# Performance work log

Measured on AMD Instinct MI355X. Metric: run time of the kernel, lower is better.

## Reference

```python
import jax, jax.numpy as jnp
import numpy as np

N = 25000        # nodes
E = 400000       # edges (before self-loops)
HEADS = 8
GROUPS = 8
F_IN = 256
HID = 64
N_CLASS = 32
N_LAYERS = 3


def grouped_linear(x, w, b):
    # x: [..., Cin], w: [G, Cin//G, Cout//G], b: [Cout]
    G = w.shape[0]
    xs = x.reshape(x.shape[:-1] + (G, -1))
    out = jnp.einsum('...gi,gio->...go', xs, w)
    return out.reshape(x.shape[:-1] + (-1,)) + b


def gcn_norm(edge_index, n):
    # PyG gcn_norm with add_self_loops=True, unit edge weights
    row = jnp.concatenate([edge_index[0], jnp.arange(n)])
    col = jnp.concatenate([edge_index[1], jnp.arange(n)])
    w = jnp.ones(row.shape[0], jnp.float32)
    deg = jax.ops.segment_sum(w, col, num_segments=n)
    dis = jnp.where(deg > 0, jax.lax.rsqrt(deg), 0.0)
    return row, col, dis[row] * w * dis[col]


def dna_conv(x_all, row, col, norm, wq, bq, wk, bk, wv, bv):
    # x_all: [N, L, H]; row/col/norm: [E'] (edges incl. self-loops)
    Ee = row.shape[0]
    L, H = x_all.shape[1], x_all.shape[2]
    dh = H // HEADS
    # query from target's latest state, key/value from full source history
    q = grouped_linear(x_all[col, -1:], wq, bq).reshape(Ee, 1, HEADS, dh).transpose(0, 2, 1, 3)
    k = grouped_linear(x_all[row], wk, bk).reshape(Ee, L, HEADS, dh).transpose(0, 2, 1, 3)
    v = grouped_linear(x_all[row], wv, bv).reshape(Ee, L, HEADS, dh).transpose(0, 2, 1, 3)
    attn = jax.nn.softmax(jnp.einsum('ehqd,ehld->ehql', q, k) / jnp.sqrt(jnp.float32(dh)), axis=-1)
    out = jnp.einsum('ehql,ehld->ehqd', attn, v)           # [E', HEADS, 1, dh]
    out = out.transpose(0, 2, 1, 3).reshape(Ee, H)          # [E', H]
    return jax.ops.segment_sum(norm[:, None] * out, col, num_segments=N)


def setup_inputs() -> dict:
    key = jax.random.key(0)
    ks = jax.random.split(key, 12)
    s = 0.2
    return {
        'x': jax.random.normal(ks[0], (N, F_IN), jnp.float32),
        'edge_index': jax.random.randint(ks[1], (2, E), 0, N),
        'lin1_w': jax.random.normal(ks[2], (F_IN, HID), jnp.float32) * 0.05,
        'lin1_b': jnp.zeros((HID,), jnp.float32),
        'wq': jax.random.normal(ks[3], (N_LAYERS, GROUPS, HID // GROUPS, HID // GROUPS), jnp.float32) * s,
        'bq': jnp.zeros((N_LAYERS, HID), jnp.float32),
        'wk': jax.random.normal(ks[4], (N_LAYERS, GROUPS, HID // GROUPS, HID // GROUPS), jnp.float32) * s,
        'bk': jnp.zeros((N_LAYERS, HID), jnp.float32),
        'wv': jax.random.normal(ks[5], (N_LAYERS, GROUPS, HID // GROUPS, HID // GROUPS), jnp.float32) * s,
        'bv': jnp.zeros((N_LAYERS, HID), jnp.float32),
        'lin2_w': jax.random.normal(ks[6], (HID, N_CLASS), jnp.float32) * 0.1,
        'lin2_b': jnp.zeros((N_CLASS,), jnp.float32),
    }


def reference(x, edge_index, lin1_w, lin1_b, wq, bq, wk, bk, wv, bv, lin2_w, lin2_b):
    row, col, norm = gcn_norm(edge_index, N)
    h = jax.nn.relu(x @ lin1_w + lin1_b)                    # [N, HID]; dropout = identity (eval)
    x_all = h[:, None, :]                                   # [N, 1, HID]
    for l in range(N_LAYERS):
        out = jax.nn.relu(dna_conv(x_all, row, col, norm,
                                   wq[l], bq[l], wk[l], bk[l], wv[l], bv[l]))
        x_all = jnp.concatenate([x_all, out[:, None, :]], axis=1)
    logits = x_all[:, -1] @ lin2_w + lin2_b                 # [N, N_CLASS]
    return jax.nn.log_softmax(logits, axis=1)
```

## Files before the change

kernel.cpp:

```cpp
#include <hip/hip_runtime.h>
#include <hip/hip_fp16.h>
#include <math.h>

#define NN 25000
#define NE 400000
#define HID 64
#define F_IN 256
#define N_CLASS 32
#define MAXL 4
#define KVS 3
#define WPAD 264
#define SCAN_NB 98

typedef _Float16 f16;
typedef _Float16 f16x2 __attribute__((ext_vector_type(2)));
typedef _Float16 f16x8 __attribute__((ext_vector_type(8)));
typedef float f32x4 __attribute__((ext_vector_type(4)));

union F16x8 {
    f16x8 v;
    f16x2 h[4];
    __half2 hh[4];
};

__device__ __forceinline__ float dot2(f16x2 a, f16x2 b, float c) {
#if __has_builtin(__builtin_amdgcn_fdot2)
    return __builtin_amdgcn_fdot2(a, b, c, false);
#else
    return c + (float)a[0] * (float)b[0] + (float)a[1] * (float)b[1];
#endif
}

__global__ void deg_kernel(const int* __restrict__ col, int* __restrict__ deg, int E) {
    int e = blockIdx.x * blockDim.x + threadIdx.x;
    if (e < E) atomicAdd(&deg[col[e]], 1);
}

__global__ void scanA_kernel(const int* __restrict__ deg, int* __restrict__ bsum, int n) {
    int t = threadIdx.x;
    int i = blockIdx.x * 256 + t;
    int v = (i < n) ? deg[i] : 0;
    #pragma unroll
    for (int off = 1; off < 64; off <<= 1) v += __shfl_xor(v, off);
    __shared__ int wsum[4];
    if ((t & 63) == 0) wsum[t >> 6] = v;
    __syncthreads();
    if (t == 0) bsum[blockIdx.x] = wsum[0] + wsum[1] + wsum[2] + wsum[3];
}

__global__ void scanB_kernel(int* __restrict__ bsum, int nb) {
    __shared__ int s[128];
    int t = threadIdx.x;
    int v = (t < nb) ? bsum[t] : 0;
    s[t] = v;
    __syncthreads();
    for (int off = 1; off < 128; off <<= 1) {
        int u = (t >= off) ? s[t - off] : 0;
        __syncthreads();
        s[t] += u;
        __syncthreads();
    }
    if (t < nb) bsum[t] = s[t] - v;
}

__global__ void scanC_kernel(const int* __restrict__ deg, const int* __restrict__ bsum,
                             int* __restrict__ rowptr, int* __restrict__ cursor,
                             float* __restrict__ dis, int n) {
    int t = threadIdx.x;
    int i = blockIdx.x * 256 + t;
    int lane = t & 63, w = t >> 6;
    int v = (i < n) ? deg[i] : 0;
    int x = v;
    #pragma unroll
    for (int off = 1; off < 64; off <<= 1) {
        int u = __shfl_up(x, off);
        if (lane >= off) x += u;
    }
    __shared__ int wsum[4];
    if (lane == 63) wsum[w] = x;
    __syncthreads();
    int base = bsum[blockIdx.x];
    for (int ww = 0; ww < w; ++ww) base += wsum[ww];
    if (i < n) {
        int excl = base + x - v;
        rowptr[i] = excl;
        cursor[i] = excl;
        dis[i] = rsqrtf((float)(v + 1));
    }
}

__global__ void scatter_kernel(const int* __restrict__ row, const int* __restrict__ col,
                               int* __restrict__ cursor, int* __restrict__ csr_src, int E) {
    int e = blockIdx.x * blockDim.x + threadIdx.x;
    if (e >= E) return;
    int c = col[e];
    int p = atomicAdd(&cursor[c], 1);
    csr_src[p] = row[e];
}

__global__ void wprep_kernel(const float* __restrict__ w, f16* __restrict__ wt) {
    int e = blockIdx.x * blockDim.x + threadIdx.x;
    int k = e >> 6, nn = e & 63;
    wt[nn * F_IN + k] = (f16)w[e];
}

__global__ void __launch_bounds__(256) lin1_mfma_kernel(
        const float* __restrict__ x, const f16x8* __restrict__ wt,
        const float* __restrict__ b, float* __restrict__ x_all, int n) {
    __shared__ f16 wlds[64 * WPAD];
    int t = threadIdx.x;
    #pragma unroll
    for (int j = 0; j < 8; ++j) {
        int idx = t + j * 256;
        int e = idx * 8;
        int nr = e >> 8, k0 = e & 255;
        *(f16x8*)&wlds[nr * WPAD + k0] = wt[idx];
    }
    __syncthreads();
    int wave = t >> 6, lane = t & 63;
    int m = lane & 15, quad = lane >> 4;
    int rowA = blockIdx.x * 64 + wave * 16 + m;
    int rA = min(rowA, n - 1);
    const float* xp = x + (size_t)rA * F_IN + quad * 8;
    f32x4 acc[4] = {};
    for (int kk = 0; kk < F_IN; kk += 32) {
        float4 x0 = *(const float4*)(xp + kk);
        float4 x1 = *(const float4*)(xp + kk + 4);
        f16x8 a;
        a[0] = (f16)x0.x; a[1] = (f16)x0.y; a[2] = (f16)x0.z; a[3] = (f16)x0.w;
        a[4] = (f16)x1.x; a[5] = (f16)x1.y; a[6] = (f16)x1.z; a[7] = (f16)x1.w;
        #pragma unroll
        for (int nt = 0; nt < 4; ++nt) {
            f16x8 bf = *(const f16x8*)&wlds[(nt * 16 + m) * WPAD + kk + quad * 8];
            acc[nt] = __builtin_amdgcn_mfma_f32_16x16x32_f16(a, bf, acc[nt], 0, 0, 0);
        }
    }
    int rowC = blockIdx.x * 64 + wave * 16 + quad * 4;
    #pragma unroll
    for (int nt = 0; nt < 4; ++nt) {
        int col = nt * 16 + m;
        float bias = b[col];
        #pragma unroll
        for (int r = 0; r < 4; ++r) {
            int row = rowC + r;
            if (row < n)
                x_all[(size_t)row * (MAXL * HID) + col] = fmaxf(acc[nt][r] + bias, 0.f);
        }
    }
}

__global__ void transform_kernel(const float* __restrict__ x_all,
                                 const float* __restrict__ wq, const float* __restrict__ bq,
                                 const float* __restrict__ wk, const float* __restrict__ bk,
                                 const float* __restrict__ wv, const float* __restrict__ bv,
                                 f16x2* __restrict__ Q2, f16x2* __restrict__ KV,
                                 int n, int L) {
    int t = blockIdx.x * blockDim.x + threadIdx.x;
    int node = t >> 5, u = t & 31;
    if (node >= n) return;
    int g = u >> 2;
    int o0 = (u & 3) * 2;
    const float* xrow = x_all + (size_t)node * (MAXL * HID);

    {
        const float* xg = xrow + (L - 1) * HID + g * 8;
        const float* wg = wq + g * 64;
        float a0 = bq[g * 8 + o0], a1 = bq[g * 8 + o0 + 1];
        #pragma unroll
        for (int i = 0; i < 8; ++i) {
            float xv = xg[i];
            a0 = fmaf(xv, wg[i * 8 + o0], a0);
            a1 = fmaf(xv, wg[i * 8 + o0 + 1], a1);
        }
        f16x2 q; q[0] = (f16)a0; q[1] = (f16)a1;
        Q2[(size_t)node * 32 + u] = q;
    }
    for (int ll = 0; ll < L; ++ll) {
        const float* xg = xrow + ll * HID + g * 8;
        const float* wgk = wk + g * 64;
        const float* wgv = wv + g * 64;
        float k0 = bk[g * 8 + o0], k1 = bk[g * 8 + o0 + 1];
        float v0 = bv[g * 8 + o0], v1 = bv[g * 8 + o0 + 1];
        #pragma unroll
        for (int i = 0; i < 8; ++i) {
            float xv = xg[i];
            k0 = fmaf(xv, wgk[i * 8 + o0], k0);
            k1 = fmaf(xv, wgk[i * 8 + o0 + 1], k1);
            v0 = fmaf(xv, wgv[i * 8 + o0], v0);
            v1 = fmaf(xv, wgv[i * 8 + o0 + 1], v1);
        }
        f16x2 kh; kh[0] = (f16)k0; kh[1] = (f16)k1;
        f16x2 vh; vh[0] = (f16)v0; vh[1] = (f16)v1;
        size_t base = ((size_t)node * KVS + ll) * 2;
        KV[(base + 0) * 32 + u] = kh;
        KV[(base + 1) * 32 + u] = vh;
    }
}

template <int L>
__global__ void gather_kernel(const int* __restrict__ rowptr, const int* __restrict__ deg,
                              const int* __restrict__ csr_src, const float* __restrict__ dis,
                              const f16x8* __restrict__ Q8, const f16x8* __restrict__ KV8,
                              float* __restrict__ x_all, int n) {
    int wave = (int)((blockIdx.x * (size_t)blockDim.x + threadIdx.x) >> 6);
    int lane = threadIdx.x & 63;
    if (wave >= n) return;
    int c = wave;
    int u = lane & 7;
    int slot = lane >> 3;
    F16x8 q; q.v = Q8[(size_t)c * 8 + u];
    float nc = dis[c];
    int beg = rowptr[c];
    int dc = deg[c] + 1;
    float acc[8];
    #pragma unroll
    for (int i = 0; i < 8; ++i) acc[i] = 0.f;

    for (int j = 0; j < dc; j += 8) {
        int jj = j + slot;
        bool valid = jj < dc;
        int r = c;
        if (valid && jj > 0) r = csr_src[beg + jj - 1];
        float nrm = valid ? nc * dis[r] : 0.f;

        F16x8 kk[L], vv[L];
        size_t rb = (size_t)r * (KVS * 2 * 8);
        #pragma unroll
        for (int ll = 0; ll < L; ++ll) {
            kk[ll].v = KV8[rb + ll * 16 + u];
            vv[ll].v = KV8[rb + ll * 16 + 8 + u];
        }
        float s[L];
        #pragma unroll
        for (int ll = 0; ll < L; ++ll) {
            float p = 0.f;
            #pragma unroll
            for (int i2 = 0; i2 < 4; ++i2) p = dot2(q.h[i2], kk[ll].h[i2], p);
            s[ll] = p * 0.35355339059327373f;
        }
        float m = s[0];
        #pragma unroll
        for (int ll = 1; ll < L; ++ll) m = fmaxf(m, s[ll]);
        float sum = 0.f;
        #pragma unroll
        for (int ll = 0; ll < L; ++ll) { s[ll] = __expf(s[ll] - m); sum += s[ll]; }
        float inv = nrm / sum;

        __half2 ha[4];
        #pragma unroll
        for (int i2 = 0; i2 < 4; ++i2) ha[i2] = __float2half2_rn(0.f);
        #pragma unroll
        for (int ll = 0; ll < L; ++ll) {
            __half2 p2 = __float2half2_rn(s[ll] * inv);
            #pragma unroll
            for (int i2 = 0; i2 < 4; ++i2) ha[i2] = __hfma2(p2, vv[ll].hh[i2], ha[i2]);
        }
        #pragma unroll
        for (int i2 = 0; i2 < 4; ++i2) {
            float2 f = __half22float2(ha[i2]);
            acc[i2 * 2]     += f.x;
            acc[i2 * 2 + 1] += f.y;
        }
    }
    #pragma unroll
    for (int off = 8; off < 64; off <<= 1) {
        #pragma unroll
        for (int i = 0; i < 8; ++i) acc[i] += __shfl_xor(acc[i], off);
    }
    if (slot == 0) {
        float4* dst = (float4*)(x_all + ((size_t)c * MAXL + L) * HID + u * 8);
        dst[0] = make_float4(fmaxf(acc[0], 0.f), fmaxf(acc[1], 0.f),
                             fmaxf(acc[2], 0.f), fmaxf(acc[3], 0.f));
        dst[1] = make_float4(fmaxf(acc[4], 0.f), fmaxf(acc[5], 0.f),
                             fmaxf(acc[6], 0.f), fmaxf(acc[7], 0.f));
    }
}

__global__ void final_kernel(const float* __restrict__ x_all, const float* __restrict__ w2,
                             const float* __restrict__ b2, float* __restrict__ out, int n) {
    int t = blockIdx.x * blockDim.x + threadIdx.x;
    int node = t >> 5;
    int o = t & 31;
    if (node >= n) return;
    const float* xr = x_all + (size_t)node * (MAXL * HID) + 3 * HID;
    float logit = b2[o];
    #pragma unroll
    for (int d = 0; d < HID; ++d) logit = fmaf(xr[d], w2[d * N_CLASS + o], logit);
    float m = logit;
    for (int off = 16; off; off >>= 1) m = fmaxf(m, __shfl_xor(m, off, 32));
    float e = expf(logit - m);
    float sum = e;
    for (int off = 16; off; off >>= 1) sum += __shfl_xor(sum, off, 32);
    out[(size_t)node * N_CLASS + o] = (logit - m) - logf(sum);
}

extern "C" void kernel_launch(void* const* d_in, const int* in_sizes, int n_in,
                              void* d_out, int out_size, void* d_ws, size_t ws_size,
                              hipStream_t stream) {
    const float* x      = (const float*)d_in[0];
    const int*   eidx   = (const int*)d_in[1];
    const float* lin1_w = (const float*)d_in[2];
    const float* lin1_b = (const float*)d_in[3];
    const float* wq     = (const float*)d_in[4];
    const float* bq     = (const float*)d_in[5];
    const float* wk     = (const float*)d_in[6];
    const float* bk     = (const float*)d_in[7];
    const float* wv     = (const float*)d_in[8];
    const float* bv     = (const float*)d_in[9];
    const float* lin2_w = (const float*)d_in[10];
    const float* lin2_b = (const float*)d_in[11];
    float* out = (float*)d_out;

    const int n  = NN;
    const int E  = NE;
    const int* row = eidx;
    const int* col = eidx + E;

    char* ws = (char*)d_ws;
    float*  x_all  = (float*)ws;   ws += (size_t)NN * MAXL * HID * 4;
    f16x2*  Q2     = (f16x2*)ws;   ws += (size_t)NN * 32 * 4;
    f16x2*  KV     = (f16x2*)ws;   ws += (size_t)NN * KVS * 2 * 32 * 4;
    float*  dis    = (float*)ws;   ws += (size_t)NN * 4;
    int*    deg    = (int*)ws;     ws += (size_t)NN * 4;
    int*    rowptr = (int*)ws;     ws += (size_t)NN * 4;
    int*    cursor = (int*)ws;     ws += (size_t)NN * 4;
    int*    csr    = (int*)ws;     ws += (size_t)NE * 4;
    f16*    wt16   = (f16*)ws;     ws += (size_t)HID * F_IN * 2;
    int*    bsum   = (int*)ws;     ws += 128 * 4;

    hipMemsetAsync(deg, 0, (size_t)NN * 4, stream);
    deg_kernel<<<(E + 255) / 256, 256, 0, stream>>>(col, deg, E);
    scanA_kernel<<<SCAN_NB, 256, 0, stream>>>(deg, bsum, n);
    scanB_kernel<<<1, 128, 0, stream>>>(bsum, SCAN_NB);
    scanC_kernel<<<SCAN_NB, 256, 0, stream>>>(deg, bsum, rowptr, cursor, dis, n);
    scatter_kernel<<<(E + 255) / 256, 256, 0, stream>>>(row, col, cursor, csr, E);
    wprep_kernel<<<(HID * F_IN + 255) / 256, 256, 0, stream>>>(lin1_w, wt16);

    lin1_mfma_kernel<<<(n + 63) / 64, 256, 0, stream>>>(x, (const f16x8*)wt16, lin1_b, x_all, n);

    for (int l = 0; l < 3; ++l) {
        int L = l + 1;
        transform_kernel<<<(n * 32 + 255) / 256, 256, 0, stream>>>(
            x_all, wq + l * 512, bq + l * 64, wk + l * 512, bk + l * 64,
            wv + l * 512, bv + l * 64, Q2, KV, n, L);
        int blocks = (n + 3) / 4;
        if (L == 1)      gather_kernel<1><<<blocks, 256, 0, stream>>>(rowptr, deg, csr, dis, (const f16x8*)Q2, (const f16x8*)KV, x_all, n);
        else if (L == 2) gather_kernel<2><<<blocks, 256, 0, stream>>>(rowptr, deg, csr, dis, (const f16x8*)Q2, (const f16x8*)KV, x_all, n);
        else             gather_kernel<3><<<blocks, 256, 0, stream>>>(rowptr, deg, csr, dis, (const f16x8*)Q2, (const f16x8*)KV, x_all, n);
    }

    final_kernel<<<(n * N_CLASS + 255) / 256, 256, 0, stream>>>(x_all, lin2_w, lin2_b, out, n);
}
```

Before: 304.5 us.

## Fuse next-layer QKV transform into gather epilogue with ping-pong buffers

Drops the separate per-layer transform kernels by computing the next layer's Q, K and V projections in the gather kernel's epilogue. Idle lanes (slots) of each wave project the new node state and the history rows into double-buffered Q/KV arrays, so the producer cannot overwrite data other waves are still reading. The gather loop also now handles two edges per slot per iteration for more memory-level parallelism, at the cost of more registers and a heavier epilogue.

```diff
diff --git a/kernel.cpp b/kernel.cpp
--- a/kernel.cpp
+++ b/kernel.cpp
@@ -149,58 +149,51 @@
     }
 }
 
-__global__ void transform_kernel(const float* __restrict__ x_all,
-                                 const float* __restrict__ wq, const float* __restrict__ bq,
-                                 const float* __restrict__ wk, const float* __restrict__ bk,
-                                 const float* __restrict__ wv, const float* __restrict__ bv,
-                                 f16x2* __restrict__ Q2, f16x2* __restrict__ KV,
-                                 int n, int L) {
+__global__ void transform0_kernel(const float* __restrict__ x_all,
+                                  const float* __restrict__ wq, const float* __restrict__ bq,
+                                  const float* __restrict__ wk, const float* __restrict__ bk,
+                                  const float* __restrict__ wv, const float* __restrict__ bv,
+                                  f16x2* __restrict__ Q2, f16x2* __restrict__ KV, int n) {
     int t = blockIdx.x * blockDim.x + threadIdx.x;
     int node = t >> 5, u = t & 31;
     if (node >= n) return;
     int g = u >> 2;
     int o0 = (u & 3) * 2;
-    const float* xrow = x_all + (size_t)node * (MAXL * HID);
-
-    {
-        const float* xg = xrow + (L - 1) * HID + g * 8;
-        const float* wg = wq + g * 64;
-        float a0 = bq[g * 8 + o0], a1 = bq[g * 8 + o0 + 1];
-        #pragma unroll
-        for (int i = 0; i < 8; ++i) {
-            float xv = xg[i];
-            a0 = fmaf(xv, wg[i * 8 + o0], a0);
-            a1 = fmaf(xv, wg[i * 8 + o0 + 1], a1);
-        }
-        f16x2 q; q[0] = (f16)a0; q[1] = (f16)a1;
-        Q2[(size_t)node * 32 + u] = q;
-    }
-    for (int ll = 0; ll < L; ++ll) {
-        const float* xg = xrow + ll * HID + g * 8;
-        const float* wgk = wk + g * 64;
-        const float* wgv = wv + g * 64;
-        float k0 = bk[g * 8 + o0], k1 = bk[g * 8 + o0 + 1];
-        float v0 = bv[g * 8 + o0], v1 = bv[g * 8 + o0 + 1];
-        #pragma unroll
-        for (int i = 0; i < 8; ++i) {
-            float xv = xg[i];
-            k0 = fmaf(xv, wgk[i * 8 + o0], k0);
-            k1 = fmaf(xv, wgk[i * 8 + o0 + 1], k1);
-            v0 = fmaf(xv, wgv[i * 8 + o0], v0);
-            v1 = fmaf(xv, wgv[i * 8 + o0 + 1], v1);
-        }
-        f16x2 kh; kh[0] = (f16)k0; kh[1] = (f16)k1;
-        f16x2 vh; vh[0] = (f16)v0; vh[1] = (f16)v1;
-        size_t base = ((size_t)node * KVS + ll) * 2;
-        KV[(base + 0) * 32 + u] = kh;
-        KV[(base + 1) * 32 + u] = vh;
-    }
-}
-
-template <int L>
+    const float* xg = x_all + (size_t)node * (MAXL * HID) + g * 8;
+
+    float a0 = bq[g * 8 + o0], a1 = bq[g * 8 + o0 + 1];
+    float k0 = bk[g * 8 + o0], k1 = bk[g * 8 + o0 + 1];
+    float v0 = bv[g * 8 + o0], v1 = bv[g * 8 + o0 + 1];
+    const float* wgq = wq + g * 64;
+    const float* wgk = wk + g * 64;
+    const float* wgv = wv + g * 64;
+    #pragma unroll
+    for (int i = 0; i < 8; ++i) {
+        float xv = xg[i];
+        a0 = fmaf(xv, wgq[i * 8 + o0], a0);
+        a1 = fmaf(xv, wgq[i * 8 + o0 + 1], a1);
+        k0 = fmaf(xv, wgk[i * 8 + o0], k0);
+        k1 = fmaf(xv, wgk[i * 8 + o0 + 1], k1);
+        v0 = fmaf(xv, wgv[i * 8 + o0], v0);
+        v1 = fmaf(xv, wgv[i * 8 + o0 + 1], v1);
+    }
+    f16x2 qh; qh[0] = (f16)a0; qh[1] = (f16)a1;
+    f16x2 kh; kh[0] = (f16)k0; kh[1] = (f16)k1;
+    f16x2 vh; vh[0] = (f16)v0; vh[1] = (f16)v1;
+    Q2[(size_t)node * 32 + u] = qh;
+    size_t base = (size_t)node * (KVS * 2);
+    KV[(base + 0) * 32 + u] = kh;
+    KV[(base + 1) * 32 + u] = vh;
+}
+
+template <int L, bool EPI>
 __global__ void gather_kernel(const int* __restrict__ rowptr, const int* __restrict__ deg,
                               const int* __restrict__ csr_src, const float* __restrict__ dis,
-                              const f16x8* __restrict__ Q8, const f16x8* __restrict__ KV8,
+                              const f16x8* __restrict__ Q8r, const f16x8* __restrict__ KV8r,
+                              f16x8* __restrict__ Q8w, f16x8* __restrict__ KV8w,
+                              const float* __restrict__ wqn, const float* __restrict__ bqn,
+                              const float* __restrict__ wkn, const float* __restrict__ bkn,
+                              const float* __restrict__ wvn, const float* __restrict__ bvn,
                               float* __restrict__ x_all, int n) {
     int wave = (int)((blockIdx.x * (size_t)blockDim.x + threadIdx.x) >> 6);
     int lane = threadIdx.x & 63;
@@ -208,7 +201,7 @@
     int c = wave;
     int u = lane & 7;
     int slot = lane >> 3;
-    F16x8 q; q.v = Q8[(size_t)c * 8 + u];
+    F16x8 q; q.v = Q8r[(size_t)c * 8 + u];
     float nc = dis[c];
     int beg = rowptr[c];
     int dc = deg[c] + 1;
@@ -216,44 +209,62 @@
     #pragma unroll
     for (int i = 0; i < 8; ++i) acc[i] = 0.f;
 
-    for (int j = 0; j < dc; j += 8) {
-        int jj = j + slot;
-        bool valid = jj < dc;
-        int r = c;
-        if (valid && jj > 0) r = csr_src[beg + jj - 1];
-        float nrm = valid ? nc * dis[r] : 0.f;
-
-        F16x8 kk[L], vv[L];
-        size_t rb = (size_t)r * (KVS * 2 * 8);
+    for (int j = 0; j < dc; j += 16) {
+        int jj0 = j + slot;
+        int jj1 = j + slot + 8;
+        bool va0 = jj0 < dc, va1 = jj1 < dc;
+        int r0 = c, r1 = c;
+        if (va0 && jj0 > 0) r0 = csr_src[beg + jj0 - 1];
+        if (va1)            r1 = csr_src[beg + jj1 - 1];
+        float nrm0 = va0 ? nc * dis[r0] : 0.f;
+        float nrm1 = va1 ? nc * dis[r1] : 0.f;
+
+        F16x8 kk0[L], vv0[L], kk1[L], vv1[L];
+        size_t rb0 = (size_t)r0 * (KVS * 2 * 8);
+        size_t rb1 = (size_t)r1 * (KVS * 2 * 8);
         #pragma unroll
         for (int ll = 0; ll < L; ++ll) {
-            kk[ll].v = KV8[rb + ll * 16 + u];
-            vv[ll].v = KV8[rb + ll * 16 + 8 + u];
-        }
-        float s[L];
+            kk0[ll].v = KV8r[rb0 + ll * 16 + u];
+            vv0[ll].v = KV8r[rb0 + ll * 16 + 8 + u];
+            kk1[ll].v = KV8r[rb1 + ll * 16 + u];
+            vv1[ll].v = KV8r[rb1 + ll * 16 + 8 + u];
+        }
+        float s0[L], s1[L];
         #pragma unroll
         for (int ll = 0; ll < L; ++ll) {
-            float p = 0.f;
+            float p0 = 0.f, p1 = 0.f;
             #pragma unroll
-            for (int i2 = 0; i2 < 4; ++i2) p = dot2(q.h[i2], kk[ll].h[i2], p);
-            s[ll] = p * 0.35355339059327373f;
-        }
-        float m = s[0];
-        #pragma unroll
-        for (int ll = 1; ll < L; ++ll) m = fmaxf(m, s[ll]);
-        float sum = 0.f;
-        #pragma unroll
-        for (int ll = 0; ll < L; ++ll) { s[ll] = __expf(s[ll] - m); sum += s[ll]; }
-        float inv = nrm / sum;
+            for (int i2 = 0; i2 < 4; ++i2) {
+                p0 = dot2(q.h[i2], kk0[ll].h[i2], p0);
+                p1 = dot2(q.h[i2], kk1[ll].h[i2], p1);
+            }
+            s0[ll] = p0 * 0.35355339059327373f;
+            s1[ll] = p1 * 0.35355339059327373f;
+        }
+        float m0 = s0[0], m1 = s1[0];
+        #pragma unroll
+        for (int ll = 1; ll < L; ++ll) { m0 = fmaxf(m0, s0[ll]); m1 = fmaxf(m1, s1[ll]); }
+        float sum0 = 0.f, sum1 = 0.f;
+        #pragma unroll
+        for (int ll = 0; ll < L; ++ll) {
+            s0[ll] = __expf(s0[ll] - m0); sum0 += s0[ll];
+            s1[ll] = __expf(s1[ll] - m1); sum1 += s1[ll];
+        }
+        float inv0 = nrm0 / sum0;
+        float inv1 = nrm1 / sum1;
 
         __half2 ha[4];
         #pragma unroll
         for (int i2 = 0; i2 < 4; ++i2) ha[i2] = __float2half2_rn(0.f);
         #pragma unroll
         for (int ll = 0; ll < L; ++ll) {
-            __half2 p2 = __float2half2_rn(s[ll] * inv);
+            __half2 p0 = __float2half2_rn(s0[ll] * inv0);
+            __half2 p1 = __float2half2_rn(s1[ll] * inv1);
             #pragma unroll
-            for (int i2 = 0; i2 < 4; ++i2) ha[i2] = __hfma2(p2, vv[ll].hh[i2], ha[i2]);
+            for (int i2 = 0; i2 < 4; ++i2) {
+                ha[i2] = __hfma2(p0, vv0[ll].hh[i2], ha[i2]);
+                ha[i2] = __hfma2(p1, vv1[ll].hh[i2], ha[i2]);
+            }
         }
         #pragma unroll
         for (int i2 = 0; i2 < 4; ++i2) {
@@ -267,12 +278,65 @@
         #pragma unroll
         for (int i = 0; i < 8; ++i) acc[i] += __shfl_xor(acc[i], off);
     }
+    float xn[8];
+    #pragma unroll
+    for (int i = 0; i < 8; ++i) xn[i] = fmaxf(acc[i], 0.f);
     if (slot == 0) {
         float4* dst = (float4*)(x_all + ((size_t)c * MAXL + L) * HID + u * 8);
-        dst[0] = make_float4(fmaxf(acc[0], 0.f), fmaxf(acc[1], 0.f),
-                             fmaxf(acc[2], 0.f), fmaxf(acc[3], 0.f));
-        dst[1] = make_float4(fmaxf(acc[4], 0.f), fmaxf(acc[5], 0.f),
-                             fmaxf(acc[6], 0.f), fmaxf(acc[7], 0.f));
+        dst[0] = make_float4(xn[0], xn[1], xn[2], xn[3]);
+        dst[1] = make_float4(xn[4], xn[5], xn[6], xn[7]);
+    }
+    if constexpr (EPI) {
+        if (slot <= L + 1) {
+            bool isQ = (slot == L + 1);
+            int s = isQ ? L : slot;
+            float xs[8];
+            if (s == L) {
+                #pragma unroll
+                for (int i = 0; i < 8; ++i) xs[i] = xn[i];
+            } else {
+                const float* xo = x_all + ((size_t)c * MAXL + s) * HID + u * 8;
+                float4 a0 = *(const float4*)xo;
+                float4 a1 = *(const float4*)(xo + 4);
+                xs[0] = a0.x; xs[1] = a0.y; xs[2] = a0.z; xs[3] = a0.w;
+                xs[4] = a1.x; xs[5] = a1.y; xs[6] = a1.z; xs[7] = a1.w;
+            }
+            if (isQ) {
+                float o[8];
+                #pragma unroll
+                for (int oo = 0; oo < 8; ++oo) o[oo] = bqn[u * 8 + oo];
+                const float* wg = wqn + u * 64;
+                #pragma unroll
+                for (int i = 0; i < 8; ++i)
+                    #pragma unroll
+                    for (int oo = 0; oo < 8; ++oo) o[oo] = fmaf(xs[i], wg[i * 8 + oo], o[oo]);
+                F16x8 pk;
+                #pragma unroll
+                for (int oo = 0; oo < 8; ++oo) pk.v[oo] = (f16)o[oo];
+                Q8w[(size_t)c * 8 + u] = pk.v;
+            } else {
+                float ok[8], ov[8];
+                #pragma unroll
+                for (int oo = 0; oo < 8; ++oo) { ok[oo] = bkn[u * 8 + oo]; ov[oo] = bvn[u * 8 + oo]; }
+                const float* wgk = wkn + u * 64;
+                const float* wgv = wvn + u * 64;
+                #pragma unroll
+                for (int i = 0; i < 8; ++i) {
+                    float xv = xs[i];
+                    #pragma unroll
+                    for (int oo = 0; oo < 8; ++oo) {
+                        ok[oo] = fmaf(xv, wgk[i * 8 + oo], ok[oo]);
+                        ov[oo] = fmaf(xv, wgv[i * 8 + oo], ov[oo]);
+                    }
+                }
+                F16x8 pk, pv;
+                #pragma unroll
+                for (int oo = 0; oo < 8; ++oo) { pk.v[oo] = (f16)ok[oo]; pv.v[oo] = (f16)ov[oo]; }
+                size_t base = (size_t)c * (KVS * 2 * 8) + s * 16;
+                KV8w[base + u]     = pk.v;
+                KV8w[base + 8 + u] = pv.v;
+            }
+        }
     }
 }
 
@@ -318,8 +382,10 @@
 
     char* ws = (char*)d_ws;
     float*  x_all  = (float*)ws;   ws += (size_t)NN * MAXL * HID * 4;
-    f16x2*  Q2     = (f16x2*)ws;   ws += (size_t)NN * 32 * 4;
-    f16x2*  KV     = (f16x2*)ws;   ws += (size_t)NN * KVS * 2 * 32 * 4;
+    f16*    Qa     = (f16*)ws;     ws += (size_t)NN * HID * 2;
+    f16*    KVa    = (f16*)ws;     ws += (size_t)NN * KVS * 2 * HID * 2;
+    f16*    Qb     = (f16*)ws;     ws += (size_t)NN * HID * 2;
+    f16*    KVb    = (f16*)ws;     ws += (size_t)NN * KVS * 2 * HID * 2;
     float*  dis    = (float*)ws;   ws += (size_t)NN * 4;
     int*    deg    = (int*)ws;     ws += (size_t)NN * 4;
     int*    rowptr = (int*)ws;     ws += (size_t)NN * 4;
@@ -338,16 +404,22 @@
 
     lin1_mfma_kernel<<<(n + 63) / 64, 256, 0, stream>>>(x, (const f16x8*)wt16, lin1_b, x_all, n);
 
-    for (int l = 0; l < 3; ++l) {
-        int L = l + 1;
-        transform_kernel<<<(n * 32 + 255) / 256, 256, 0, stream>>>(
-            x_all, wq + l * 512, bq + l * 64, wk + l * 512, bk + l * 64,
-            wv + l * 512, bv + l * 64, Q2, KV, n, L);
-        int blocks = (n + 3) / 4;
-        if (L == 1)      gather_kernel<1><<<blocks, 256, 0, stream>>>(rowptr, deg, csr, dis, (const f16x8*)Q2, (const f16x8*)KV, x_all, n);
-        else if (L == 2) gather_kernel<2><<<blocks, 256, 0, stream>>>(rowptr, deg, csr, dis, (const f16x8*)Q2, (const f16x8*)KV, x_all, n);
-        else             gather_kernel<3><<<blocks, 256, 0, stream>>>(rowptr, deg, csr, dis, (const f16x8*)Q2, (const f16x8*)KV, x_all, n);
-    }
+    transform0_kernel<<<(n * 32 + 255) / 256, 256, 0, stream>>>(
+        x_all, wq, bq, wk, bk, wv, bv, (f16x2*)Qa, (f16x2*)KVa, n);
+
+    int blocks = (n + 3) / 4;
+    gather_kernel<1, true><<<blocks, 256, 0, stream>>>(
+        rowptr, deg, csr, dis, (const f16x8*)Qa, (const f16x8*)KVa,
+        (f16x8*)Qb, (f16x8*)KVb,
+        wq + 512, bq + 64, wk + 512, bk + 64, wv + 512, bv + 64, x_all, n);
+    gather_kernel<2, true><<<blocks, 256, 0, stream>>>(
+        rowptr, deg, csr, dis, (const f16x8*)Qb, (const f16x8*)KVb,
+        (f16x8*)Qa, (f16x8*)KVa,
+        wq + 1024, bq + 128, wk + 1024, bk + 128, wv + 1024, bv + 128, x_all, n);
+    gather_kernel<3, false><<<blocks, 256, 0, stream>>>(
+        rowptr, deg, csr, dis, (const f16x8*)Qa, (const f16x8*)KVa,
+        (f16x8*)Qb, (f16x8*)KVb,
+        wq, bq, wk, bk, wv, bv, x_all, n);
 
     final_kernel<<<(n * N_CLASS + 255) / 256, 256, 0, stream>>>(x_all, lin2_w, lin2_b, out, n);
 }
```

Measured after the change: 373.7 us. +22.7%, slower.

## Fold source degree norm into V and process two edges per lane per iteration

Applied to the files above, without the earlier changes.

The source-side normalization dis[r] is folded into V in the transform kernel, and the target-side dis[c] is applied once at output. This removes the per-edge dis[r] gather. The gather loop now handles two edges per lane slot (16 per iteration), so more independent loads are in flight to hide memory latency. The cost is more registers per lane, which could lower occupancy, and V now holds pre-scaled fp16 values.

```diff
diff --git a/kernel.cpp b/kernel.cpp
--- a/kernel.cpp
+++ b/kernel.cpp
@@ -153,6 +153,7 @@
                                  const float* __restrict__ wq, const float* __restrict__ bq,
                                  const float* __restrict__ wk, const float* __restrict__ bk,
                                  const float* __restrict__ wv, const float* __restrict__ bv,
+                                 const float* __restrict__ dis,
                                  f16x2* __restrict__ Q2, f16x2* __restrict__ KV,
                                  int n, int L) {
     int t = blockIdx.x * blockDim.x + threadIdx.x;
@@ -161,6 +162,7 @@
     int g = u >> 2;
     int o0 = (u & 3) * 2;
     const float* xrow = x_all + (size_t)node * (MAXL * HID);
+    float d = dis[node];
 
     {
         const float* xg = xrow + (L - 1) * HID + g * 8;
@@ -190,7 +192,7 @@
             v1 = fmaf(xv, wgv[i * 8 + o0 + 1], v1);
         }
         f16x2 kh; kh[0] = (f16)k0; kh[1] = (f16)k1;
-        f16x2 vh; vh[0] = (f16)v0; vh[1] = (f16)v1;
+        f16x2 vh; vh[0] = (f16)(v0 * d); vh[1] = (f16)(v1 * d);
         size_t base = ((size_t)node * KVS + ll) * 2;
         KV[(base + 0) * 32 + u] = kh;
         KV[(base + 1) * 32 + u] = vh;
@@ -216,44 +218,60 @@
     #pragma unroll
     for (int i = 0; i < 8; ++i) acc[i] = 0.f;
 
-    for (int j = 0; j < dc; j += 8) {
-        int jj = j + slot;
-        bool valid = jj < dc;
-        int r = c;
-        if (valid && jj > 0) r = csr_src[beg + jj - 1];
-        float nrm = valid ? nc * dis[r] : 0.f;
-
-        F16x8 kk[L], vv[L];
-        size_t rb = (size_t)r * (KVS * 2 * 8);
+    for (int j = 0; j < dc; j += 16) {
+        int jj0 = j + slot;
+        int jj1 = j + slot + 8;
+        bool va0 = jj0 < dc, va1 = jj1 < dc;
+        int r0 = c, r1 = c;
+        if (va0 && jj0 > 0) r0 = csr_src[beg + jj0 - 1];
+        if (va1)            r1 = csr_src[beg + jj1 - 1];
+
+        F16x8 kk0[L], vv0[L], kk1[L], vv1[L];
+        size_t rb0 = (size_t)r0 * (KVS * 2 * 8);
+        size_t rb1 = (size_t)r1 * (KVS * 2 * 8);
         #pragma unroll
         for (int ll = 0; ll < L; ++ll) {
-            kk[ll].v = KV8[rb + ll * 16 + u];
-            vv[ll].v = KV8[rb + ll * 16 + 8 + u];
-        }
-        float s[L];
+            kk0[ll].v = KV8[rb0 + ll * 16 + u];
+            vv0[ll].v = KV8[rb0 + ll * 16 + 8 + u];
+            kk1[ll].v = KV8[rb1 + ll * 16 + u];
+            vv1[ll].v = KV8[rb1 + ll * 16 + 8 + u];
+        }
+        float s0[L], s1[L];
         #pragma unroll
         for (int ll = 0; ll < L; ++ll) {
-            float p = 0.f;
+            float p0 = 0.f, p1 = 0.f;
             #pragma unroll
-            for (int i2 = 0; i2 < 4; ++i2) p = dot2(q.h[i2], kk[ll].h[i2], p);
-            s[ll] = p * 0.35355339059327373f;
-        }
-        float m = s[0];
-        #pragma unroll
-        for (int ll = 1; ll < L; ++ll) m = fmaxf(m, s[ll]);
-        float sum = 0.f;
-        #pragma unroll
-        for (int ll = 0; ll < L; ++ll) { s[ll] = __expf(s[ll] - m); sum += s[ll]; }
-        float inv = nrm / sum;
+            for (int i2 = 0; i2 < 4; ++i2) {
+                p0 = dot2(q.h[i2], kk0[ll].h[i2], p0);
+                p1 = dot2(q.h[i2], kk1[ll].h[i2], p1);
+            }
+            s0[ll] = p0 * 0.35355339059327373f;
+            s1[ll] = p1 * 0.35355339059327373f;
+        }
+        float m0 = s0[0], m1 = s1[0];
+        #pragma unroll
+        for (int ll = 1; ll < L; ++ll) { m0 = fmaxf(m0, s0[ll]); m1 = fmaxf(m1, s1[ll]); }
+        float sum0 = 0.f, sum1 = 0.f;
+        #pragma unroll
+        for (int ll = 0; ll < L; ++ll) {
+            s0[ll] = __expf(s0[ll] - m0); sum0 += s0[ll];
+            s1[ll] = __expf(s1[ll] - m1); sum1 += s1[ll];
+        }
+        float inv0 = va0 ? 1.f / sum0 : 0.f;
+        float inv1 = va1 ? 1.f / sum1 : 0.f;
 
         __half2 ha[4];
         #pragma unroll
         for (int i2 = 0; i2 < 4; ++i2) ha[i2] = __float2half2_rn(0.f);
         #pragma unroll
         for (int ll = 0; ll < L; ++ll) {
-            __half2 p2 = __float2half2_rn(s[ll] * inv);
+            __half2 p0 = __float2half2_rn(s0[ll] * inv0);
+            __half2 p1 = __float2half2_rn(s1[ll] * inv1);
             #pragma unroll
-            for (int i2 = 0; i2 < 4; ++i2) ha[i2] = __hfma2(p2, vv[ll].hh[i2], ha[i2]);
+            for (int i2 = 0; i2 < 4; ++i2) {
+                ha[i2] = __hfma2(p0, vv0[ll].hh[i2], ha[i2]);
+                ha[i2] = __hfma2(p1, vv1[ll].hh[i2], ha[i2]);
+            }
         }
         #pragma unroll
         for (int i2 = 0; i2 < 4; ++i2) {
@@ -269,10 +287,10 @@
     }
     if (slot == 0) {
         float4* dst = (float4*)(x_all + ((size_t)c * MAXL + L) * HID + u * 8);
-        dst[0] = make_float4(fmaxf(acc[0], 0.f), fmaxf(acc[1], 0.f),
-                             fmaxf(acc[2], 0.f), fmaxf(acc[3], 0.f));
-        dst[1] = make_float4(fmaxf(acc[4], 0.f), fmaxf(acc[5], 0.f),
-                             fmaxf(acc[6], 0.f), fmaxf(acc[7], 0.f));
+        dst[0] = make_float4(fmaxf(acc[0] * nc, 0.f), fmaxf(acc[1] * nc, 0.f),
+                             fmaxf(acc[2] * nc, 0.f), fmaxf(acc[3] * nc, 0.f));
+        dst[1] = make_float4(fmaxf(acc[4] * nc, 0.f), fmaxf(acc[5] * nc, 0.f),
+                             fmaxf(acc[6] * nc, 0.f), fmaxf(acc[7] * nc, 0.f));
     }
 }
 
@@ -342,7 +360,7 @@
         int L = l + 1;
         transform_kernel<<<(n * 32 + 255) / 256, 256, 0, stream>>>(
             x_all, wq + l * 512, bq + l * 64, wk + l * 512, bk + l * 64,
-            wv + l * 512, bv + l * 64, Q2, KV, n, L);
+            wv + l * 512, bv + l * 64, dis, Q2, KV, n, L);
         int blocks = (n + 3) / 4;
         if (L == 1)      gather_kernel<1><<<blocks, 256, 0, stream>>>(rowptr, deg, csr, dis, (const f16x8*)Q2, (const f16x8*)KV, x_all, n);
         else if (L == 2) gather_kernel<2><<<blocks, 256, 0, stream>>>(rowptr, deg, csr, dis, (const f16x8*)Q2, (const f16x8*)KV, x_all, n);
```

Measured after the change: 297.8 us. 1.02x faster.
